# Optimization experiments

Measured on AMD Instinct MI355X. Metric: run time of the kernel, lower is better.

The kernel has to match this reference:

```python
import jax, jax.numpy as jnp
import numpy as np

OBS_LEN = 8
PRED_LEN = 12
BATCH = 65536
EMB = 64
H = 64


def setup_inputs() -> dict:
    key = jax.random.key(0)
    ks = jax.random.split(key, 18)
    s = 1.0 / np.sqrt(H)  # torch default uniform bound scale, used as std here

    def p(k, shape):
        return (jax.random.normal(k, shape, dtype=jnp.float32) * s).astype(jnp.float32)

    return {
        "obs_traj": jax.random.normal(ks[0], (OBS_LEN, BATCH, 2), dtype=jnp.float32),
        "obs_traj_rel": jax.random.normal(ks[1], (OBS_LEN, BATCH, 2), dtype=jnp.float32),
        # encoder params
        "enc_emb_w": p(ks[2], (EMB, 2)),
        "enc_emb_b": p(ks[3], (EMB,)),
        "enc_w_ih": p(ks[4], (4 * H, EMB)),
        "enc_w_hh": p(ks[5], (4 * H, H)),
        "enc_b_ih": p(ks[6], (4 * H,)),
        "enc_b_hh": p(ks[7], (4 * H,)),
        # decoder params
        "dec_emb_w": p(ks[8], (EMB, 2)),
        "dec_emb_b": p(ks[9], (EMB,)),
        "dec_w_ih": p(ks[10], (4 * H, EMB)),
        "dec_w_hh": p(ks[11], (4 * H, H)),
        "dec_b_ih": p(ks[12], (4 * H,)),
        "dec_b_hh": p(ks[13], (4 * H,)),
        "h2p_w": p(ks[14], (2, H)),
        "h2p_b": p(ks[15], (2,)),
    }


def _lstm_cell(h, c, x, w_ih, w_hh, b_ih, b_hh):
    # torch nn.LSTM gate order: i, f, g, o
    gates = x @ w_ih.T + h @ w_hh.T + (b_ih + b_hh)
    i, f, g, o = jnp.split(gates, 4, axis=-1)
    c_new = jax.nn.sigmoid(f) * c + jax.nn.sigmoid(i) * jnp.tanh(g)
    h_new = jax.nn.sigmoid(o) * jnp.tanh(c_new)
    return h_new, c_new


def reference(obs_traj, obs_traj_rel,
              enc_emb_w, enc_emb_b, enc_w_ih, enc_w_hh, enc_b_ih, enc_b_hh,
              dec_emb_w, dec_emb_b, dec_w_ih, dec_w_hh, dec_b_ih, dec_b_hh,
              h2p_w, h2p_b):
    batch = obs_traj_rel.shape[1]

    # ---------- Encoder ----------
    enc_in = obs_traj_rel @ enc_emb_w.T + enc_emb_b  # [T, B, EMB]

    def enc_step(carry, x_t):
        h, c = carry
        h, c = _lstm_cell(h, c, x_t, enc_w_ih, enc_w_hh, enc_b_ih, enc_b_hh)
        return (h, c), None

    h0 = jnp.zeros((batch, H), dtype=obs_traj_rel.dtype)
    c0 = jnp.zeros((batch, H), dtype=obs_traj_rel.dtype)
    (h_enc, _), _ = jax.lax.scan(enc_step, (h0, c0), enc_in)

    # ---------- Decoder ----------
    dec_h = h_enc                                   # final encoder hidden seeds decoder
    dec_c = jnp.zeros((batch, H), dtype=obs_traj_rel.dtype)
    last_pos_rel = obs_traj_rel[-1]
    dec_in = last_pos_rel @ dec_emb_w.T + dec_emb_b  # [B, EMB]

    def dec_step(carry, _):
        h, c, x = carry
        h, c = _lstm_cell(h, c, x, dec_w_ih, dec_w_hh, dec_b_ih, dec_b_hh)
        rel_pos = h @ h2p_w.T + h2p_b               # [B, 2]
        x_next = rel_pos @ dec_emb_w.T + dec_emb_b  # [B, EMB]
        return (h, c, x_next), rel_pos

    (_, _, _), pred_traj_fake_rel = jax.lax.scan(
        dec_step, (dec_h, dec_c, dec_in), None, length=PRED_LEN)
    return pred_traj_fake_rel  # [PRED_LEN, B, 2]
```

## Files before the change

kernel.cpp:

```cpp
#include <hip/hip_runtime.h>

#define OBS_LEN 8
#define PRED_LEN 12
#define TILE_B 64
#define NTHREADS 256
#define HSTR 72

typedef __attribute__((ext_vector_type(8))) short short8;
typedef __attribute__((ext_vector_type(4))) float floatx4;
typedef __attribute__((ext_vector_type(2))) float floatx2;
typedef __attribute__((ext_vector_type(4))) unsigned short ushortx4;
typedef __attribute__((ext_vector_type(2))) unsigned int u32x2;
typedef unsigned short u16;
typedef unsigned int u32;

#define L2E 1.442695040888963f

__device__ __forceinline__ u16 f2bf(float f) {
  __bf16 b = (__bf16)f;
  return __builtin_bit_cast(u16, b);
}
__device__ __forceinline__ float bf2f(u16 h) {
  return __builtin_bit_cast(float, ((u32)h) << 16);
}
__device__ __forceinline__ float rndbf(float f) { return (float)(__bf16)f; }

#if __has_builtin(__builtin_amdgcn_exp2f)
__device__ __forceinline__ float fexp2_(float x) { return __builtin_amdgcn_exp2f(x); }
#else
__device__ __forceinline__ float fexp2_(float x) { return exp2f(x); }
#endif
__device__ __forceinline__ floatx2 exp2v(floatx2 x) {
  floatx2 r;
  r.x = fexp2_(x.x);
  r.y = fexp2_(x.y);
  return r;
}
#if __has_builtin(__builtin_amdgcn_rcpf)
__device__ __forceinline__ floatx2 rcp2(floatx2 x) {
  floatx2 r;
  r.x = __builtin_amdgcn_rcpf(x.x);
  r.y = __builtin_amdgcn_rcpf(x.y);
  return r * (2.0f - x * r);
}
#else
__device__ __forceinline__ floatx2 rcp2(floatx2 x) {
  return floatx2{1.0f / x.x, 1.0f / x.y};
}
#endif

__device__ __forceinline__ floatx4 mfma_bf(short8 a, short8 b, floatx4 c) {
  return __builtin_amdgcn_mfma_f32_16x16x32_bf16(a, b, c, 0, 0, 0);
}

__device__ __forceinline__ void load_afrags(const float* __restrict__ W,
                                            short8 (&af)[4][2],
                                            int u0, int q, int l16) {
#pragma unroll
  for (int t = 0; t < 4; ++t)
#pragma unroll
    for (int kf = 0; kf < 2; ++kf) {
      const float* src = W + (t * 64 + u0 + l16) * 64 + kf * 32 + q * 8;
      const floatx4 w0 = *(const floatx4*)src;
      const floatx4 w1 = *(const floatx4*)(src + 4);
      short8 a;
#pragma unroll
      for (int j = 0; j < 4; ++j) {
        a[j] = (short)f2bf(w0[j]);
        a[j + 4] = (short)f2bf(w1[j]);
      }
      af[t][kf] = a;
    }
}

__device__ __forceinline__ void cell_step(const u16* __restrict__ rdh,
                                          const u16* __restrict__ rdx,
                                          u16* __restrict__ wrh,
                                          const short8 (&afh)[4][2],
                                          const short8 (&afx)[4][2],
                                          const floatx4 (&bacc)[4],
                                          floatx2 (&c)[4][2],
                                          int q, int l16, int u0) {
#pragma unroll
  for (int n = 0; n < 4; ++n) {
    const int s = n * 16 + l16;
    const short8 hb0 = *(const short8*)(rdh + s * HSTR + q * 8);
    const short8 hb1 = *(const short8*)(rdh + s * HSTR + 32 + q * 8);
    const short8 xb0 = *(const short8*)(rdx + s * HSTR + q * 8);
    const short8 xb1 = *(const short8*)(rdx + s * HSTR + 32 + q * 8);
    floatx4 acc[4];
#pragma unroll
    for (int t = 0; t < 4; ++t) acc[t] = mfma_bf(afh[t][0], hb0, bacc[t]);
#pragma unroll
    for (int t = 0; t < 4; ++t) acc[t] = mfma_bf(afx[t][0], xb0, acc[t]);
#pragma unroll
    for (int t = 0; t < 4; ++t) acc[t] = mfma_bf(afh[t][1], hb1, acc[t]);
#pragma unroll
    for (int t = 0; t < 4; ++t) acc[t] = mfma_bf(afx[t][1], xb1, acc[t]);
    u32 hpk[2];
#pragma unroll
    for (int p = 0; p < 2; ++p) {
      const floatx2 iv = {acc[0][2 * p], acc[0][2 * p + 1]};
      const floatx2 fv = {acc[1][2 * p], acc[1][2 * p + 1]};
      const floatx2 gv = {acc[2][2 * p], acc[2][2 * p + 1]};
      const floatx2 ov = {acc[3][2 * p], acc[3][2 * p + 1]};
      const floatx2 ei = exp2v(iv * -L2E);
      const floatx2 ef = exp2v(fv * -L2E);
      const floatx2 eg = exp2v(gv * (2.0f * L2E));
      const floatx2 eo = exp2v(ov * -L2E);
      const floatx2 A = ei + 1.0f;
      const floatx2 F = ef + 1.0f;
      const floatx2 Bg = eg + 1.0f;
      const floatx2 P = A * Bg;
      const floatx2 num = c[n][p] * P + (eg - 1.0f) * F;
      const floatx2 cn = num * rcp2(F * P);
      c[n][p] = cn;
      const floatx2 ec = exp2v(cn * (2.0f * L2E));
      const floatx2 h = (ec - 1.0f) * rcp2((eo + 1.0f) * (ec + 1.0f));
      hpk[p] = (u32)f2bf(h.x) | ((u32)f2bf(h.y) << 16);
    }
    *(u32x2*)(wrh + s * HSTR + u0 + q * 4) = u32x2{hpk[0], hpk[1]};
  }
}

__device__ __forceinline__ void xgen16(float rb0, float rb1,
                                       const float* __restrict__ ew0,
                                       const float* __restrict__ ew1,
                                       const float* __restrict__ eb,
                                       u16* __restrict__ xw, int s, int p) {
#pragma unroll
  for (int i4 = 0; i4 < 4; ++i4) {
    const int e = p * 16 + i4 * 4;
    const floatx2 wa0 = *(const floatx2*)(ew0 + e);
    const floatx2 wa1 = *(const floatx2*)(ew0 + e + 2);
    const floatx2 wb0 = *(const floatx2*)(ew1 + e);
    const floatx2 wb1 = *(const floatx2*)(ew1 + e + 2);
    const floatx2 ba0 = *(const floatx2*)(eb + e);
    const floatx2 ba1 = *(const floatx2*)(eb + e + 2);
    const floatx2 x0 = wa0 * rb0 + (wb0 * rb1 + ba0);
    const floatx2 x1 = wa1 * rb0 + (wb1 * rb1 + ba1);
    const u32x2 pk = {(u32)f2bf(x0.x) | ((u32)f2bf(x0.y) << 16),
                      (u32)f2bf(x1.x) | ((u32)f2bf(x1.y) << 16)};
    *(u32x2*)(xw + s * HSTR + e) = pk;
  }
}

__device__ __forceinline__ void areldot(const u16* __restrict__ h,
                                        const floatx2* __restrict__ hwp,
                                        float b2p0, float b2p1, int s, int p,
                                        float& r0, float& r1) {
  floatx2 d = {0.f, 0.f};
#pragma unroll
  for (int i4 = 0; i4 < 4; ++i4) {
    const ushortx4 hv4 = *(const ushortx4*)(h + s * HSTR + p * 16 + i4 * 4);
#pragma unroll
    for (int ii = 0; ii < 4; ++ii) {
      const int u = p * 16 + i4 * 4 + ii;
      d = hwp[u] * bf2f(hv4[ii]) + d;
    }
  }
  d.x += __shfl_xor(d.x, 1);
  d.x += __shfl_xor(d.x, 2);
  d.y += __shfl_xor(d.y, 1);
  d.y += __shfl_xor(d.y, 2);
  r0 = d.x + b2p0;
  r1 = d.y + b2p1;
}

__global__ void __launch_bounds__(NTHREADS, 3)
lstm_kernel(const float* __restrict__ obs_rel,
            const float* __restrict__ enc_emb_w, const float* __restrict__ enc_emb_b,
            const float* __restrict__ enc_w_ih, const float* __restrict__ enc_w_hh,
            const float* __restrict__ enc_b_ih, const float* __restrict__ enc_b_hh,
            const float* __restrict__ dec_emb_w, const float* __restrict__ dec_emb_b,
            const float* __restrict__ dec_w_ih, const float* __restrict__ dec_w_hh,
            const float* __restrict__ dec_b_ih, const float* __restrict__ dec_b_hh,
            const float* __restrict__ h2p_w, const float* __restrict__ h2p_b,
            float* __restrict__ out, int batch) {
  __shared__ __align__(16) u16 hS[2][TILE_B * HSTR];
  __shared__ __align__(16) u16 xS[2][TILE_B * HSTR];
  __shared__ float ew0e[64], ew1e[64], ebe[64];
  __shared__ float ew0d[64], ew1d[64], ebd[64];
  __shared__ __align__(8) floatx2 hwp[64];

  const int tid = threadIdx.x;
  const int wv = tid >> 6, lane = tid & 63;
  const int q = lane >> 4, l16 = lane & 15;
  const int u0 = wv << 4;
  const int s4 = tid >> 2, p4 = tid & 3;
  const long S0 = (long)blockIdx.x * TILE_B;

  if (tid < 64) {
    ew0e[tid] = rndbf(enc_emb_w[tid * 2]);
    ew1e[tid] = rndbf(enc_emb_w[tid * 2 + 1]);
    ebe[tid] = enc_emb_b[tid];
    ew0d[tid] = rndbf(dec_emb_w[tid * 2]);
    ew1d[tid] = rndbf(dec_emb_w[tid * 2 + 1]);
    ebd[tid] = dec_emb_b[tid];
    hwp[tid] = floatx2{rndbf(h2p_w[tid]), rndbf(h2p_w[64 + tid])};
  }
  for (int i = tid; i < TILE_B * HSTR / 2; i += NTHREADS) ((u32*)&hS[0][0])[i] = 0;

  short8 afh[4][2], afx[4][2];
  floatx4 bacc[4];
  floatx2 c[4][2];
  load_afrags(enc_w_hh, afh, u0, q, l16);
  load_afrags(enc_w_ih, afx, u0, q, l16);
#pragma unroll
  for (int t = 0; t < 4; ++t) {
#pragma unroll
    for (int r = 0; r < 4; ++r) {
      const int g = t * 64 + u0 + q * 4 + r;
      bacc[t][r] = enc_b_ih[g] + enc_b_hh[g];
    }
  }
#pragma unroll
  for (int n = 0; n < 4; ++n) c[n][0] = c[n][1] = floatx2{0.f, 0.f};
  const float b2p0 = h2p_b[0], b2p1 = h2p_b[1];
  __syncthreads();
  {
    const floatx2 rr = *(const floatx2*)(obs_rel + (S0 + s4) * 2);
    xgen16(rndbf(rr.x), rndbf(rr.y), ew0e, ew1e, ebe, xS[0], s4, p4);
  }
  __syncthreads();

  int pb = 0;
#pragma unroll 1
  for (int t = 0; t < OBS_LEN; ++t) {
    const int tn = t + 1;
    const float* orow = obs_rel + (long)((tn < 8) ? tn : 7) * batch * 2 + S0 * 2;
    const floatx2 rr = *(const floatx2*)(orow + s4 * 2);
    if (tn < 8)
      xgen16(rndbf(rr.x), rndbf(rr.y), ew0e, ew1e, ebe, xS[tn & 1], s4, p4);
    else
      xgen16(rndbf(rr.x), rndbf(rr.y), ew0d, ew1d, ebd, xS[0], s4, p4);
    cell_step(hS[pb], xS[t & 1], hS[pb ^ 1], afh, afx, bacc, c, q, l16, u0);
    __syncthreads();
    pb ^= 1;
  }

  load_afrags(dec_w_hh, afh, u0, q, l16);
  load_afrags(dec_w_ih, afx, u0, q, l16);
#pragma unroll
  for (int t = 0; t < 4; ++t) {
#pragma unroll
    for (int r = 0; r < 4; ++r) {
      const int g = t * 64 + u0 + q * 4 + r;
      bacc[t][r] = dec_b_ih[g] + dec_b_hh[g];
    }
  }
#pragma unroll
  for (int n = 0; n < 4; ++n) c[n][0] = c[n][1] = floatx2{0.f, 0.f};
  cell_step(hS[pb], xS[0], hS[pb ^ 1], afh, afx, bacc, c, q, l16, u0);
  __syncthreads();
  pb ^= 1;

#pragma unroll 1
  for (int j = 1; j < PRED_LEN; ++j) {
    float r0, r1;
    areldot(hS[pb], hwp, b2p0, b2p1, s4, p4, r0, r1);
    if (p4 == 0)
      *(floatx2*)(out + (long)(j - 1) * batch * 2 + (S0 + s4) * 2) = floatx2{r0, r1};
    xgen16(rndbf(r0), rndbf(r1), ew0d, ew1d, ebd, xS[0], s4, p4);
    __syncthreads();
    cell_step(hS[pb], xS[0], hS[pb ^ 1], afh, afx, bacc, c, q, l16, u0);
    __syncthreads();
    pb ^= 1;
  }

  {
    float r0, r1;
    areldot(hS[pb], hwp, b2p0, b2p1, s4, p4, r0, r1);
    if (p4 == 0)
      *(floatx2*)(out + (long)(PRED_LEN - 1) * batch * 2 + (S0 + s4) * 2) =
          floatx2{r0, r1};
  }
}

extern "C" void kernel_launch(void* const* d_in, const int* in_sizes, int n_in,
                              void* d_out, int out_size, void* d_ws, size_t ws_size,
                              hipStream_t stream) {
  const float* obs_rel = (const float*)d_in[1];
  const int batch = in_sizes[1] / (OBS_LEN * 2);

  const int blocks = batch / TILE_B;
  hipLaunchKernelGGL(lstm_kernel, dim3(blocks), dim3(NTHREADS), 0, stream,
                     obs_rel,
                     (const float*)d_in[2], (const float*)d_in[3],
                     (const float*)d_in[4], (const float*)d_in[5],
                     (const float*)d_in[6], (const float*)d_in[7],
                     (const float*)d_in[8], (const float*)d_in[9],
                     (const float*)d_in[10], (const float*)d_in[11],
                     (const float*)d_in[12], (const float*)d_in[13],
                     (const float*)d_in[14], (const float*)d_in[15],
                     (float*)d_out, batch);
}
```

Baseline: 240.7 us.

## Fuse input embedding and h2p projection into LSTM step, drop x buffers

Builds the embedded input in registers per MFMA B-fragment instead of writing it to a shared-memory x buffer, and computes the hidden-to-position projection with a small MFMA directly in the step. This removes one barrier per decoder step and the separate xS buffers. Observations are prefetched into shared memory up front, and the first encoder step skips the zero-hidden matmuls. In exchange every wave recomputes the embedding redundantly, and each step still relies on cross-lane shuffles and the MFMA result layout being correct.

```diff
diff --git a/kernel.cpp b/kernel.cpp
--- a/kernel.cpp
+++ b/kernel.cpp
@@ -9,7 +9,6 @@
 typedef __attribute__((ext_vector_type(8))) short short8;
 typedef __attribute__((ext_vector_type(4))) float floatx4;
 typedef __attribute__((ext_vector_type(2))) float floatx2;
-typedef __attribute__((ext_vector_type(4))) unsigned short ushortx4;
 typedef __attribute__((ext_vector_type(2))) unsigned int u32x2;
 typedef unsigned short u16;
 typedef unsigned int u32;
@@ -73,28 +72,67 @@
     }
 }
 
-__device__ __forceinline__ void cell_step(const u16* __restrict__ rdh,
-                                          const u16* __restrict__ rdx,
-                                          u16* __restrict__ wrh,
-                                          const short8 (&afh)[4][2],
-                                          const short8 (&afx)[4][2],
-                                          const floatx4 (&bacc)[4],
-                                          floatx2 (&c)[4][2],
-                                          int q, int l16, int u0) {
+template <bool HASH, bool REL>
+__device__ __forceinline__ void lstm_step(
+    const u16* __restrict__ rdh, u16* __restrict__ wrh,
+    const float* __restrict__ posrow,
+    const short8 (&afh)[4][2], const short8 (&afx)[4][2],
+    const short8 (&aex)[2],
+    const float* __restrict__ biasrow,
+    const u16* __restrict__ ew0, const u16* __restrict__ ew1,
+    const float* __restrict__ eb,
+    floatx2 (&c)[4][2],
+    float* __restrict__ outp, float b2p0, float b2p1,
+    int q, int l16, int u0) {
+  const short8 e0a = *(const short8*)(ew0 + q * 8);
+  const short8 e0b = *(const short8*)(ew0 + 32 + q * 8);
+  const short8 e1a = *(const short8*)(ew1 + q * 8);
+  const short8 e1b = *(const short8*)(ew1 + 32 + q * 8);
 #pragma unroll
   for (int n = 0; n < 4; ++n) {
     const int s = n * 16 + l16;
-    const short8 hb0 = *(const short8*)(rdh + s * HSTR + q * 8);
-    const short8 hb1 = *(const short8*)(rdh + s * HSTR + 32 + q * 8);
-    const short8 xb0 = *(const short8*)(rdx + s * HSTR + q * 8);
-    const short8 xb1 = *(const short8*)(rdx + s * HSTR + 32 + q * 8);
+    short8 hb0, hb1;
+    if (HASH) {
+      hb0 = *(const short8*)(rdh + s * HSTR + q * 8);
+      hb1 = *(const short8*)(rdh + s * HSTR + 32 + q * 8);
+    }
+    float rb0, rb1;
+    if (REL) {
+      floatx4 z = {0.f, 0.f, 0.f, 0.f};
+      z = mfma_bf(aex[0], hb0, z);
+      z = mfma_bf(aex[1], hb1, z);
+      if (q == 0)
+        *(floatx2*)(outp + s * 2) = floatx2{z[0] + b2p0, z[1] + b2p1};
+      rb0 = rndbf(__shfl(z[0], l16) + b2p0);
+      rb1 = rndbf(__shfl(z[1], l16) + b2p1);
+    } else {
+      const floatx2 rr = *(const floatx2*)(posrow + s * 2);
+      rb0 = rndbf(rr.x);
+      rb1 = rndbf(rr.y);
+    }
+    short8 xb0, xb1;
+#pragma unroll
+    for (int j = 0; j < 8; ++j) {
+      const float x0 =
+          rb0 * bf2f((u16)e0a[j]) + (rb1 * bf2f((u16)e1a[j]) + eb[q * 8 + j]);
+      const float x1 = rb0 * bf2f((u16)e0b[j]) +
+                       (rb1 * bf2f((u16)e1b[j]) + eb[32 + q * 8 + j]);
+      xb0[j] = (short)f2bf(x0);
+      xb1[j] = (short)f2bf(x1);
+    }
     floatx4 acc[4];
 #pragma unroll
-    for (int t = 0; t < 4; ++t) acc[t] = mfma_bf(afh[t][0], hb0, bacc[t]);
-#pragma unroll
-    for (int t = 0; t < 4; ++t) acc[t] = mfma_bf(afx[t][0], xb0, acc[t]);
-#pragma unroll
-    for (int t = 0; t < 4; ++t) acc[t] = mfma_bf(afh[t][1], hb1, acc[t]);
+    for (int t = 0; t < 4; ++t) {
+      const floatx4 bias = *(const floatx4*)(biasrow + t * 64 + u0 + q * 4);
+      acc[t] = HASH ? mfma_bf(afh[t][0], hb0, bias)
+                    : mfma_bf(afx[t][0], xb0, bias);
+    }
+    if (HASH) {
+#pragma unroll
+      for (int t = 0; t < 4; ++t) acc[t] = mfma_bf(afx[t][0], xb0, acc[t]);
+#pragma unroll
+      for (int t = 0; t < 4; ++t) acc[t] = mfma_bf(afh[t][1], hb1, acc[t]);
+    }
 #pragma unroll
     for (int t = 0; t < 4; ++t) acc[t] = mfma_bf(afx[t][1], xb1, acc[t]);
     u32 hpk[2];
@@ -121,50 +159,7 @@
     }
     *(u32x2*)(wrh + s * HSTR + u0 + q * 4) = u32x2{hpk[0], hpk[1]};
   }
-}
-
-__device__ __forceinline__ void xgen16(float rb0, float rb1,
-                                       const float* __restrict__ ew0,
-                                       const float* __restrict__ ew1,
-                                       const float* __restrict__ eb,
-                                       u16* __restrict__ xw, int s, int p) {
-#pragma unroll
-  for (int i4 = 0; i4 < 4; ++i4) {
-    const int e = p * 16 + i4 * 4;
-    const floatx2 wa0 = *(const floatx2*)(ew0 + e);
-    const floatx2 wa1 = *(const floatx2*)(ew0 + e + 2);
-    const floatx2 wb0 = *(const floatx2*)(ew1 + e);
-    const floatx2 wb1 = *(const floatx2*)(ew1 + e + 2);
-    const floatx2 ba0 = *(const floatx2*)(eb + e);
-    const floatx2 ba1 = *(const floatx2*)(eb + e + 2);
-    const floatx2 x0 = wa0 * rb0 + (wb0 * rb1 + ba0);
-    const floatx2 x1 = wa1 * rb0 + (wb1 * rb1 + ba1);
-    const u32x2 pk = {(u32)f2bf(x0.x) | ((u32)f2bf(x0.y) << 16),
-                      (u32)f2bf(x1.x) | ((u32)f2bf(x1.y) << 16)};
-    *(u32x2*)(xw + s * HSTR + e) = pk;
-  }
-}
-
-__device__ __forceinline__ void areldot(const u16* __restrict__ h,
-                                        const floatx2* __restrict__ hwp,
-                                        float b2p0, float b2p1, int s, int p,
-                                        float& r0, float& r1) {
-  floatx2 d = {0.f, 0.f};
-#pragma unroll
-  for (int i4 = 0; i4 < 4; ++i4) {
-    const ushortx4 hv4 = *(const ushortx4*)(h + s * HSTR + p * 16 + i4 * 4);
-#pragma unroll
-    for (int ii = 0; ii < 4; ++ii) {
-      const int u = p * 16 + i4 * 4 + ii;
-      d = hwp[u] * bf2f(hv4[ii]) + d;
-    }
-  }
-  d.x += __shfl_xor(d.x, 1);
-  d.x += __shfl_xor(d.x, 2);
-  d.y += __shfl_xor(d.y, 1);
-  d.y += __shfl_xor(d.y, 2);
-  r0 = d.x + b2p0;
-  r1 = d.y + b2p1;
+  __syncthreads();
 }
 
 __global__ void __launch_bounds__(NTHREADS, 3)
@@ -178,102 +173,96 @@
             const float* __restrict__ h2p_w, const float* __restrict__ h2p_b,
             float* __restrict__ out, int batch) {
   __shared__ __align__(16) u16 hS[2][TILE_B * HSTR];
-  __shared__ __align__(16) u16 xS[2][TILE_B * HSTR];
-  __shared__ float ew0e[64], ew1e[64], ebe[64];
-  __shared__ float ew0d[64], ew1d[64], ebd[64];
-  __shared__ __align__(8) floatx2 hwp[64];
+  __shared__ __align__(16) float posS[OBS_LEN][TILE_B * 2];
+  __shared__ __align__(16) u16 ewpk[4][64];
+  __shared__ __align__(16) float ebS[2][64];
+  __shared__ __align__(16) float biasS[2][256];
 
   const int tid = threadIdx.x;
   const int wv = tid >> 6, lane = tid & 63;
   const int q = lane >> 4, l16 = lane & 15;
   const int u0 = wv << 4;
-  const int s4 = tid >> 2, p4 = tid & 3;
   const long S0 = (long)blockIdx.x * TILE_B;
 
+  {
+    const int t = tid >> 5, i = tid & 31;
+    *(floatx4*)&posS[t][i * 4] =
+        *(const floatx4*)(obs_rel + (long)t * batch * 2 + S0 * 2 + i * 4);
+  }
   if (tid < 64) {
-    ew0e[tid] = rndbf(enc_emb_w[tid * 2]);
-    ew1e[tid] = rndbf(enc_emb_w[tid * 2 + 1]);
-    ebe[tid] = enc_emb_b[tid];
-    ew0d[tid] = rndbf(dec_emb_w[tid * 2]);
-    ew1d[tid] = rndbf(dec_emb_w[tid * 2 + 1]);
-    ebd[tid] = dec_emb_b[tid];
-    hwp[tid] = floatx2{rndbf(h2p_w[tid]), rndbf(h2p_w[64 + tid])};
-  }
-  for (int i = tid; i < TILE_B * HSTR / 2; i += NTHREADS) ((u32*)&hS[0][0])[i] = 0;
-
-  short8 afh[4][2], afx[4][2];
-  floatx4 bacc[4];
+    ewpk[0][tid] = f2bf(enc_emb_w[tid * 2]);
+    ewpk[1][tid] = f2bf(enc_emb_w[tid * 2 + 1]);
+    ewpk[2][tid] = f2bf(dec_emb_w[tid * 2]);
+    ewpk[3][tid] = f2bf(dec_emb_w[tid * 2 + 1]);
+    ebS[0][tid] = enc_emb_b[tid];
+    ebS[1][tid] = dec_emb_b[tid];
+  }
+  biasS[0][tid] = enc_b_ih[tid] + enc_b_hh[tid];
+  biasS[1][tid] = dec_b_ih[tid] + dec_b_hh[tid];
+
+  short8 afh[4][2], afx[4][2], aex[2];
   floatx2 c[4][2];
   load_afrags(enc_w_hh, afh, u0, q, l16);
   load_afrags(enc_w_ih, afx, u0, q, l16);
 #pragma unroll
-  for (int t = 0; t < 4; ++t) {
-#pragma unroll
-    for (int r = 0; r < 4; ++r) {
-      const int g = t * 64 + u0 + q * 4 + r;
-      bacc[t][r] = enc_b_ih[g] + enc_b_hh[g];
-    }
-  }
-#pragma unroll
   for (int n = 0; n < 4; ++n) c[n][0] = c[n][1] = floatx2{0.f, 0.f};
   const float b2p0 = h2p_b[0], b2p1 = h2p_b[1];
   __syncthreads();
-  {
-    const floatx2 rr = *(const floatx2*)(obs_rel + (S0 + s4) * 2);
-    xgen16(rndbf(rr.x), rndbf(rr.y), ew0e, ew1e, ebe, xS[0], s4, p4);
-  }
-  __syncthreads();
-
+
+  lstm_step<false, false>(hS[0], hS[0], posS[0], afh, afx, aex, biasS[0],
+                          ewpk[0], ewpk[1], ebS[0], c, nullptr, b2p0, b2p1,
+                          q, l16, u0);
   int pb = 0;
 #pragma unroll 1
-  for (int t = 0; t < OBS_LEN; ++t) {
-    const int tn = t + 1;
-    const float* orow = obs_rel + (long)((tn < 8) ? tn : 7) * batch * 2 + S0 * 2;
-    const floatx2 rr = *(const floatx2*)(orow + s4 * 2);
-    if (tn < 8)
-      xgen16(rndbf(rr.x), rndbf(rr.y), ew0e, ew1e, ebe, xS[tn & 1], s4, p4);
-    else
-      xgen16(rndbf(rr.x), rndbf(rr.y), ew0d, ew1d, ebd, xS[0], s4, p4);
-    cell_step(hS[pb], xS[t & 1], hS[pb ^ 1], afh, afx, bacc, c, q, l16, u0);
-    __syncthreads();
+  for (int t = 1; t < OBS_LEN; ++t) {
+    lstm_step<true, false>(hS[pb], hS[pb ^ 1], posS[t], afh, afx, aex, biasS[0],
+                           ewpk[0], ewpk[1], ebS[0], c, nullptr, b2p0, b2p1,
+                           q, l16, u0);
     pb ^= 1;
   }
 
   load_afrags(dec_w_hh, afh, u0, q, l16);
   load_afrags(dec_w_ih, afx, u0, q, l16);
 #pragma unroll
-  for (int t = 0; t < 4; ++t) {
-#pragma unroll
-    for (int r = 0; r < 4; ++r) {
-      const int g = t * 64 + u0 + q * 4 + r;
-      bacc[t][r] = dec_b_ih[g] + dec_b_hh[g];
-    }
+  for (int kf = 0; kf < 2; ++kf) {
+    short8 a = {0, 0, 0, 0, 0, 0, 0, 0};
+    if (l16 < 2) {
+      const float* src = h2p_w + l16 * 64 + kf * 32 + q * 8;
+#pragma unroll
+      for (int j = 0; j < 8; ++j) a[j] = (short)f2bf(src[j]);
+    }
+    aex[kf] = a;
   }
 #pragma unroll
   for (int n = 0; n < 4; ++n) c[n][0] = c[n][1] = floatx2{0.f, 0.f};
-  cell_step(hS[pb], xS[0], hS[pb ^ 1], afh, afx, bacc, c, q, l16, u0);
-  __syncthreads();
+
+  lstm_step<true, false>(hS[pb], hS[pb ^ 1], posS[7], afh, afx, aex, biasS[1],
+                         ewpk[2], ewpk[3], ebS[1], c, nullptr, b2p0, b2p1,
+                         q, l16, u0);
   pb ^= 1;
 
 #pragma unroll 1
   for (int j = 1; j < PRED_LEN; ++j) {
-    float r0, r1;
-    areldot(hS[pb], hwp, b2p0, b2p1, s4, p4, r0, r1);
-    if (p4 == 0)
-      *(floatx2*)(out + (long)(j - 1) * batch * 2 + (S0 + s4) * 2) = floatx2{r0, r1};
-    xgen16(rndbf(r0), rndbf(r1), ew0d, ew1d, ebd, xS[0], s4, p4);
-    __syncthreads();
-    cell_step(hS[pb], xS[0], hS[pb ^ 1], afh, afx, bacc, c, q, l16, u0);
-    __syncthreads();
+    lstm_step<true, true>(hS[pb], hS[pb ^ 1], nullptr, afh, afx, aex, biasS[1],
+                          ewpk[2], ewpk[3], ebS[1], c,
+                          out + (long)(j - 1) * batch * 2 + S0 * 2, b2p0, b2p1,
+                          q, l16, u0);
     pb ^= 1;
   }
 
   {
-    float r0, r1;
-    areldot(hS[pb], hwp, b2p0, b2p1, s4, p4, r0, r1);
-    if (p4 == 0)
-      *(floatx2*)(out + (long)(PRED_LEN - 1) * batch * 2 + (S0 + s4) * 2) =
-          floatx2{r0, r1};
+    float* outp = out + (long)(PRED_LEN - 1) * batch * 2 + S0 * 2;
+#pragma unroll
+    for (int n = 0; n < 4; ++n) {
+      const int s = n * 16 + l16;
+      const short8 hb0 = *(const short8*)(&hS[pb][0] + s * HSTR + q * 8);
+      const short8 hb1 = *(const short8*)(&hS[pb][0] + s * HSTR + 32 + q * 8);
+      floatx4 z = {0.f, 0.f, 0.f, 0.f};
+      z = mfma_bf(aex[0], hb0, z);
+      z = mfma_bf(aex[1], hb1, z);
+      if (q == 0)
+        *(floatx2*)(outp + s * 2) = floatx2{z[0] + b2p0, z[1] + b2p1};
+    }
   }
 }
 
```

New measurement: 352.9 us. +46.6%, slower.

## Halve batch tile, XOR-swizzle LDS layout, preload positions, drop rcp Newton step

Applied to the files above, without the earlier changes.

Batch tile per block drops from 64 to 32, so the block count doubles and each wave handles two column fragments instead of four. The launch-bounds occupancy hint rises from 3 to 4. The padded LDS rows are replaced by an XOR-swizzled 64-wide layout to avoid bank conflicts. The embedding and readout steps are remapped to 8 threads per sample, with an extra shuffle step. Observed positions are staged in shared memory up front, and the Newton refinement after the hardware reciprocal is removed, which lowers accuracy slightly. Each block now amortises the weight-fragment loads over fewer samples.

```diff
diff --git a/kernel.cpp b/kernel.cpp
--- a/kernel.cpp
+++ b/kernel.cpp
@@ -2,14 +2,12 @@
 
 #define OBS_LEN 8
 #define PRED_LEN 12
-#define TILE_B 64
+#define TILE_B 32
 #define NTHREADS 256
-#define HSTR 72
 
 typedef __attribute__((ext_vector_type(8))) short short8;
 typedef __attribute__((ext_vector_type(4))) float floatx4;
 typedef __attribute__((ext_vector_type(2))) float floatx2;
-typedef __attribute__((ext_vector_type(4))) unsigned short ushortx4;
 typedef __attribute__((ext_vector_type(2))) unsigned int u32x2;
 typedef unsigned short u16;
 typedef unsigned int u32;
@@ -41,7 +39,7 @@
   floatx2 r;
   r.x = __builtin_amdgcn_rcpf(x.x);
   r.y = __builtin_amdgcn_rcpf(x.y);
-  return r * (2.0f - x * r);
+  return r;
 }
 #else
 __device__ __forceinline__ floatx2 rcp2(floatx2 x) {
@@ -51,6 +49,10 @@
 
 __device__ __forceinline__ floatx4 mfma_bf(short8 a, short8 b, floatx4 c) {
   return __builtin_amdgcn_mfma_f32_16x16x32_bf16(a, b, c, 0, 0, 0);
+}
+
+__device__ __forceinline__ int swz(int s, int b) {
+  return s * 64 + ((b ^ (s & 7)) * 8);
 }
 
 __device__ __forceinline__ void load_afrags(const float* __restrict__ W,
@@ -79,15 +81,18 @@
                                           const short8 (&afh)[4][2],
                                           const short8 (&afx)[4][2],
                                           const floatx4 (&bacc)[4],
-                                          floatx2 (&c)[4][2],
-                                          int q, int l16, int u0) {
-#pragma unroll
-  for (int n = 0; n < 4; ++n) {
+                                          floatx2 (&c)[2][2],
+                                          int q, int l16, int wv) {
+#pragma unroll
+  for (int n = 0; n < 2; ++n) {
     const int s = n * 16 + l16;
-    const short8 hb0 = *(const short8*)(rdh + s * HSTR + q * 8);
-    const short8 hb1 = *(const short8*)(rdh + s * HSTR + 32 + q * 8);
-    const short8 xb0 = *(const short8*)(rdx + s * HSTR + q * 8);
-    const short8 xb1 = *(const short8*)(rdx + s * HSTR + 32 + q * 8);
+    const int sw = s & 7;
+    const u16* hr = rdh + s * 64;
+    const u16* xr = rdx + s * 64;
+    const short8 hb0 = *(const short8*)(hr + ((q ^ sw) * 8));
+    const short8 hb1 = *(const short8*)(hr + (((q + 4) ^ sw) * 8));
+    const short8 xb0 = *(const short8*)(xr + ((q ^ sw) * 8));
+    const short8 xb1 = *(const short8*)(xr + (((q + 4) ^ sw) * 8));
     floatx4 acc[4];
 #pragma unroll
     for (int t = 0; t < 4; ++t) acc[t] = mfma_bf(afh[t][0], hb0, bacc[t]);
@@ -119,55 +124,44 @@
       const floatx2 h = (ec - 1.0f) * rcp2((eo + 1.0f) * (ec + 1.0f));
       hpk[p] = (u32)f2bf(h.x) | ((u32)f2bf(h.y) << 16);
     }
-    *(u32x2*)(wrh + s * HSTR + u0 + q * 4) = u32x2{hpk[0], hpk[1]};
-  }
-}
-
-__device__ __forceinline__ void xgen16(float rb0, float rb1,
-                                       const float* __restrict__ ew0,
-                                       const float* __restrict__ ew1,
-                                       const float* __restrict__ eb,
-                                       u16* __restrict__ xw, int s, int p) {
-#pragma unroll
-  for (int i4 = 0; i4 < 4; ++i4) {
-    const int e = p * 16 + i4 * 4;
-    const floatx2 wa0 = *(const floatx2*)(ew0 + e);
-    const floatx2 wa1 = *(const floatx2*)(ew0 + e + 2);
-    const floatx2 wb0 = *(const floatx2*)(ew1 + e);
-    const floatx2 wb1 = *(const floatx2*)(ew1 + e + 2);
-    const floatx2 ba0 = *(const floatx2*)(eb + e);
-    const floatx2 ba1 = *(const floatx2*)(eb + e + 2);
-    const floatx2 x0 = wa0 * rb0 + (wb0 * rb1 + ba0);
-    const floatx2 x1 = wa1 * rb0 + (wb1 * rb1 + ba1);
-    const u32x2 pk = {(u32)f2bf(x0.x) | ((u32)f2bf(x0.y) << 16),
-                      (u32)f2bf(x1.x) | ((u32)f2bf(x1.y) << 16)};
-    *(u32x2*)(xw + s * HSTR + e) = pk;
-  }
+    *(u32x2*)(wrh + s * 64 + (((wv * 2 + (q >> 1)) ^ sw) * 8) + (q & 1) * 4) =
+        u32x2{hpk[0], hpk[1]};
+  }
+}
+
+__device__ __forceinline__ void xgen8(float rb0, float rb1,
+                                      const float* __restrict__ ew0,
+                                      const float* __restrict__ ew1,
+                                      const float* __restrict__ eb,
+                                      u16* __restrict__ xw, int s8, int p8) {
+  short8 v;
+#pragma unroll
+  for (int j = 0; j < 8; ++j) {
+    const int e = p8 * 8 + j;
+    v[j] = (short)f2bf(rb0 * ew0[e] + (rb1 * ew1[e] + eb[e]));
+  }
+  *(short8*)(xw + swz(s8, p8)) = v;
 }
 
 __device__ __forceinline__ void areldot(const u16* __restrict__ h,
                                         const floatx2* __restrict__ hwp,
-                                        float b2p0, float b2p1, int s, int p,
+                                        float b2p0, float b2p1, int s8, int p8,
                                         float& r0, float& r1) {
+  const short8 hv = *(const short8*)(h + swz(s8, p8));
   floatx2 d = {0.f, 0.f};
 #pragma unroll
-  for (int i4 = 0; i4 < 4; ++i4) {
-    const ushortx4 hv4 = *(const ushortx4*)(h + s * HSTR + p * 16 + i4 * 4);
-#pragma unroll
-    for (int ii = 0; ii < 4; ++ii) {
-      const int u = p * 16 + i4 * 4 + ii;
-      d = hwp[u] * bf2f(hv4[ii]) + d;
-    }
-  }
+  for (int j = 0; j < 8; ++j) d = hwp[p8 * 8 + j] * bf2f((u16)hv[j]) + d;
   d.x += __shfl_xor(d.x, 1);
   d.x += __shfl_xor(d.x, 2);
+  d.x += __shfl_xor(d.x, 4);
   d.y += __shfl_xor(d.y, 1);
   d.y += __shfl_xor(d.y, 2);
+  d.y += __shfl_xor(d.y, 4);
   r0 = d.x + b2p0;
   r1 = d.y + b2p1;
 }
 
-__global__ void __launch_bounds__(NTHREADS, 3)
+__global__ void __launch_bounds__(NTHREADS, 4)
 lstm_kernel(const float* __restrict__ obs_rel,
             const float* __restrict__ enc_emb_w, const float* __restrict__ enc_emb_b,
             const float* __restrict__ enc_w_ih, const float* __restrict__ enc_w_hh,
@@ -177,8 +171,9 @@
             const float* __restrict__ dec_b_ih, const float* __restrict__ dec_b_hh,
             const float* __restrict__ h2p_w, const float* __restrict__ h2p_b,
             float* __restrict__ out, int batch) {
-  __shared__ __align__(16) u16 hS[2][TILE_B * HSTR];
-  __shared__ __align__(16) u16 xS[2][TILE_B * HSTR];
+  __shared__ __align__(16) u16 hS[2][TILE_B * 64];
+  __shared__ __align__(16) u16 xS[2][TILE_B * 64];
+  __shared__ __align__(16) float posS[OBS_LEN][TILE_B * 2];
   __shared__ float ew0e[64], ew1e[64], ebe[64];
   __shared__ float ew0d[64], ew1d[64], ebd[64];
   __shared__ __align__(8) floatx2 hwp[64];
@@ -187,9 +182,14 @@
   const int wv = tid >> 6, lane = tid & 63;
   const int q = lane >> 4, l16 = lane & 15;
   const int u0 = wv << 4;
-  const int s4 = tid >> 2, p4 = tid & 3;
+  const int s8 = tid >> 3, p8 = tid & 7;
   const long S0 = (long)blockIdx.x * TILE_B;
 
+  if (tid < 128) {
+    const int t = tid >> 4, i = tid & 15;
+    *(floatx4*)&posS[t][i * 4] =
+        *(const floatx4*)(obs_rel + (long)t * batch * 2 + S0 * 2 + i * 4);
+  }
   if (tid < 64) {
     ew0e[tid] = rndbf(enc_emb_w[tid * 2]);
     ew1e[tid] = rndbf(enc_emb_w[tid * 2 + 1]);
@@ -199,28 +199,26 @@
     ebd[tid] = dec_emb_b[tid];
     hwp[tid] = floatx2{rndbf(h2p_w[tid]), rndbf(h2p_w[64 + tid])};
   }
-  for (int i = tid; i < TILE_B * HSTR / 2; i += NTHREADS) ((u32*)&hS[0][0])[i] = 0;
+  for (int i = tid; i < TILE_B * 64 / 2; i += NTHREADS) ((u32*)&hS[0][0])[i] = 0;
 
   short8 afh[4][2], afx[4][2];
   floatx4 bacc[4];
-  floatx2 c[4][2];
+  floatx2 c[2][2];
   load_afrags(enc_w_hh, afh, u0, q, l16);
   load_afrags(enc_w_ih, afx, u0, q, l16);
 #pragma unroll
-  for (int t = 0; t < 4; ++t) {
+  for (int t = 0; t < 4; ++t)
 #pragma unroll
     for (int r = 0; r < 4; ++r) {
       const int g = t * 64 + u0 + q * 4 + r;
       bacc[t][r] = enc_b_ih[g] + enc_b_hh[g];
     }
-  }
-#pragma unroll
-  for (int n = 0; n < 4; ++n) c[n][0] = c[n][1] = floatx2{0.f, 0.f};
+  c[0][0] = c[0][1] = c[1][0] = c[1][1] = floatx2{0.f, 0.f};
   const float b2p0 = h2p_b[0], b2p1 = h2p_b[1];
   __syncthreads();
   {
-    const floatx2 rr = *(const floatx2*)(obs_rel + (S0 + s4) * 2);
-    xgen16(rndbf(rr.x), rndbf(rr.y), ew0e, ew1e, ebe, xS[0], s4, p4);
+    const floatx2 rr = *(const floatx2*)(&posS[0][s8 * 2]);
+    xgen8(rndbf(rr.x), rndbf(rr.y), ew0e, ew1e, ebe, xS[0], s8, p8);
   }
   __syncthreads();
 
@@ -228,13 +226,12 @@
 #pragma unroll 1
   for (int t = 0; t < OBS_LEN; ++t) {
     const int tn = t + 1;
-    const float* orow = obs_rel + (long)((tn < 8) ? tn : 7) * batch * 2 + S0 * 2;
-    const floatx2 rr = *(const floatx2*)(orow + s4 * 2);
+    const floatx2 rr = *(const floatx2*)(&posS[(tn < 8) ? tn : 7][s8 * 2]);
     if (tn < 8)
-      xgen16(rndbf(rr.x), rndbf(rr.y), ew0e, ew1e, ebe, xS[tn & 1], s4, p4);
+      xgen8(rndbf(rr.x), rndbf(rr.y), ew0e, ew1e, ebe, xS[tn & 1], s8, p8);
     else
-      xgen16(rndbf(rr.x), rndbf(rr.y), ew0d, ew1d, ebd, xS[0], s4, p4);
-    cell_step(hS[pb], xS[t & 1], hS[pb ^ 1], afh, afx, bacc, c, q, l16, u0);
+      xgen8(rndbf(rr.x), rndbf(rr.y), ew0d, ew1d, ebd, xS[0], s8, p8);
+    cell_step(hS[pb], xS[t & 1], hS[pb ^ 1], afh, afx, bacc, c, q, l16, wv);
     __syncthreads();
     pb ^= 1;
   }
@@ -242,37 +239,35 @@
   load_afrags(dec_w_hh, afh, u0, q, l16);
   load_afrags(dec_w_ih, afx, u0, q, l16);
 #pragma unroll
-  for (int t = 0; t < 4; ++t) {
+  for (int t = 0; t < 4; ++t)
 #pragma unroll
     for (int r = 0; r < 4; ++r) {
       const int g = t * 64 + u0 + q * 4 + r;
       bacc[t][r] = dec_b_ih[g] + dec_b_hh[g];
     }
-  }
-#pragma unroll
-  for (int n = 0; n < 4; ++n) c[n][0] = c[n][1] = floatx2{0.f, 0.f};
-  cell_step(hS[pb], xS[0], hS[pb ^ 1], afh, afx, bacc, c, q, l16, u0);
+  c[0][0] = c[0][1] = c[1][0] = c[1][1] = floatx2{0.f, 0.f};
+  cell_step(hS[pb], xS[0], hS[pb ^ 1], afh, afx, bacc, c, q, l16, wv);
   __syncthreads();
   pb ^= 1;
 
 #pragma unroll 1
   for (int j = 1; j < PRED_LEN; ++j) {
     float r0, r1;
-    areldot(hS[pb], hwp, b2p0, b2p1, s4, p4, r0, r1);
-    if (p4 == 0)
-      *(floatx2*)(out + (long)(j - 1) * batch * 2 + (S0 + s4) * 2) = floatx2{r0, r1};
-    xgen16(rndbf(r0), rndbf(r1), ew0d, ew1d, ebd, xS[0], s4, p4);
+    areldot(hS[pb], hwp, b2p0, b2p1, s8, p8, r0, r1);
+    if (p8 == 0)
+      *(floatx2*)(out + (long)(j - 1) * batch * 2 + (S0 + s8) * 2) = floatx2{r0, r1};
+    xgen8(rndbf(r0), rndbf(r1), ew0d, ew1d, ebd, xS[0], s8, p8);
     __syncthreads();
-    cell_step(hS[pb], xS[0], hS[pb ^ 1], afh, afx, bacc, c, q, l16, u0);
+    cell_step(hS[pb], xS[0], hS[pb ^ 1], afh, afx, bacc, c, q, l16, wv);
     __syncthreads();
     pb ^= 1;
   }
 
   {
     float r0, r1;
-    areldot(hS[pb], hwp, b2p0, b2p1, s4, p4, r0, r1);
-    if (p4 == 0)
-      *(floatx2*)(out + (long)(PRED_LEN - 1) * batch * 2 + (S0 + s4) * 2) =
+    areldot(hS[pb], hwp, b2p0, b2p1, s8, p8, r0, r1);
+    if (p8 == 0)
+      *(floatx2*)(out + (long)(PRED_LEN - 1) * batch * 2 + (S0 + s8) * 2) =
           floatx2{r0, r1};
   }
 }
```

Measured after the change: 265.6 us. 1.1x slower.
